# Kernel tuning notes

Measured on AMD Instinct MI355X. Metric: run time of the kernel, lower is better.

## Reference

```python
import jax, jax.numpy as jnp
import numpy as np

NUM_HEADS = 16


def setup_inputs() -> dict:
    key = jax.random.key(0)
    ks = jax.random.split(key, 7)
    T, B, E = 2048, 2, 1024
    return {
        "query": jax.random.normal(ks[0], (T, B, E), jnp.float32),
        "key": jax.random.normal(ks[1], (T, B, E), jnp.float32),
        "value": jax.random.normal(ks[2], (T, B, E), jnp.float32),
        "query_pos": jax.random.normal(ks[3], (T, B, E), jnp.float32),
        "key_pos": jax.random.normal(ks[4], (T, B, E), jnp.float32),
        "W": jax.random.normal(ks[5], (E, E), jnp.float32) * (1.0 / np.sqrt(E)),
        "b": jax.random.normal(ks[6], (E,), jnp.float32) * 0.01,
    }


def reference(query, key, value, query_pos, key_pos, W, b):
    T, B, E = query.shape
    S = key.shape[0]
    H = NUM_HEADS
    D = E // H
    scale = jnp.asarray(D ** 0.5, query.dtype)

    identity = query  # residual uses query BEFORE positional add
    q = query + query_pos
    k = key + key_pos

    # (T,B,E) -> (B,H,T,D)
    q = q.reshape(T, B, H, D).transpose(1, 2, 0, 3)
    k = k.reshape(S, B, H, D).transpose(1, 2, 0, 3)
    v = value.reshape(S, B, H, D).transpose(1, 2, 0, 3)

    attn = jnp.einsum("bhtd,bhsd->bhts", q, k) / scale
    attn = jax.nn.softmax(attn, axis=-1)  # dropout p=0 -> identity

    out = jnp.einsum("bhts,bhsd->bhtd", attn, v)
    out = out.transpose(2, 0, 1, 3).reshape(T, B, E)  # (B,H,T,D)->(T,B,E)
    out = out @ W.T + b  # fuse_heads linear; out_dropout p=0 -> identity
    out = out + identity

    attn_avg = attn.sum(axis=1) / H  # average over heads -> (B,T,S)
    return out, attn_avg
```

## Files before the change

kernel.cpp:

```cpp
#include <hip/hip_runtime.h>

#define T_DIM 2048
#define S_DIM 2048
#define B_DIM 2
#define E_DIM 1024
#define H_DIM 16
#define D_DIM 64
#define MSHIFT 20.0f

typedef unsigned short u16;
typedef unsigned int u32;
typedef float v4f __attribute__((ext_vector_type(4)));
typedef short v8s __attribute__((ext_vector_type(8)));

__device__ __forceinline__ u16 f2bf(float f) {
    union { float f; u32 u; } x; x.f = f;
    return (u16)((x.u + 0x7fffu + ((x.u >> 16) & 1u)) >> 16);
}
__device__ __forceinline__ u16 f2bfr(float f) {
    union { float f; u32 u; } x; x.f = f;
    return (u16)((x.u + 0x8000u) >> 16);
}
__device__ __forceinline__ v4f mfma16(v8s a, v8s b, v4f c) {
    return __builtin_amdgcn_mfma_f32_16x16x32_bf16(a, b, c, 0, 0, 0);
}
__device__ __forceinline__ v8s ld8(const u16* p) {
    return *reinterpret_cast<const v8s*>(p);
}

__global__ __launch_bounds__(256) void prep_qk(
    const float* __restrict__ q, const float* __restrict__ qp,
    const float* __restrict__ k, const float* __restrict__ kp,
    u16* __restrict__ qb, u16* __restrict__ ks) {
    int o = blockIdx.x * 256 + threadIdx.x;
    int d = o & 63, t = (o >> 6) & 2047, h = (o >> 17) & 15, b = o >> 21;
    int src = ((t * B_DIM + b) << 10) + (h << 6) + d;
    qb[o] = f2bf(q[src] + qp[src]);
    ks[o] = f2bf(k[src] + kp[src]);
}

__global__ __launch_bounds__(256) void prep_w(const float* __restrict__ W, u16* __restrict__ Wb) {
    int o = blockIdx.x * 256 + threadIdx.x;
    Wb[o] = f2bf(W[o]);
}

__global__ __launch_bounds__(256) void prep_vt(const float* __restrict__ V, u16* __restrict__ vt) {
    __shared__ float tile[64 * 65];
    int bx = blockIdx.x;
    int bh = bx >> 5;
    int s0 = (bx & 31) * 64;
    int b = bh >> 4, h = bh & 15;
    int tid = threadIdx.x;
    int quarter = tid >> 6, c = tid & 63;
    int boff = b * E_DIM + h * 64;
#pragma unroll
    for (int p = 0; p < 16; ++p) {
        int r = quarter * 16 + p;
        tile[r * 65 + c] = V[(size_t)(s0 + r) * (B_DIM * E_DIM) + boff + c];
    }
    __syncthreads();
#pragma unroll
    for (int p = 0; p < 16; ++p) {
        int d = quarter * 16 + p;
        vt[(size_t)bh * (D_DIM * S_DIM) + (size_t)d * S_DIM + s0 + c] = f2bf(tile[c * 65 + d]);
    }
}

#define PITCH 72
__global__ __launch_bounds__(256) void attn_pv(
    const u16* __restrict__ qb, const u16* __restrict__ ks, const u16* __restrict__ vt,
    float* __restrict__ lin, u16* __restrict__ Xb) {
    __shared__ u16 Kl[2][64 * PITCH];
    __shared__ u16 Vl[2][64 * PITCH];
    __shared__ u16 Pl[4][32 * PITCH];

    int bx = blockIdx.x;
    int bh = bx >> 4;
    int b = bh >> 4, h = bh & 15;
    int tid = threadIdx.x;
    int w = tid >> 6;
    int tbase = (bx & 15) * 128 + w * 32;
    int lane = tid & 63;
    int m = lane & 15, g = lane >> 4;

    int srow = tid >> 2;
    int sqtr = (tid & 3) * 16;

    uint4 kr0, kr1, vr0, vr1;
    auto load_stage = [&](int s0) {
        const uint4* kp = reinterpret_cast<const uint4*>(
            ks + ((size_t)bh * S_DIM + s0 + srow) * 64 + sqtr);
        kr0 = kp[0]; kr1 = kp[1];
        const uint4* vp = reinterpret_cast<const uint4*>(
            vt + (size_t)bh * (D_DIM * S_DIM) + (size_t)srow * S_DIM + s0 + sqtr);
        vr0 = vp[0]; vr1 = vp[1];
    };
    auto write_stage = [&](int buf) {
        uint4* kd = reinterpret_cast<uint4*>(&Kl[buf][srow * PITCH + sqtr]);
        kd[0] = kr0; kd[1] = kr1;
        uint4* vd = reinterpret_cast<uint4*>(&Vl[buf][srow * PITCH + sqtr]);
        vd[0] = vr0; vd[1] = vr1;
    };

    const u16* qrow = qb + ((size_t)bh * T_DIM + tbase + m) * 64 + g * 8;
    v8s aq[2][2];
    aq[0][0] = ld8(qrow);        aq[0][1] = ld8(qrow + 32);
    aq[1][0] = ld8(qrow + 1024); aq[1][1] = ld8(qrow + 1024 + 32);

    v4f O[2][4];
    float lacc[2][4];
#pragma unroll
    for (int tr = 0; tr < 2; ++tr) {
#pragma unroll
        for (int dd = 0; dd < 4; ++dd) O[tr][dd] = (v4f){0.f, 0.f, 0.f, 0.f};
#pragma unroll
        for (int r = 0; r < 4; ++r) lacc[tr][r] = 0.f;
    }

    load_stage(0);
    write_stage(0);
    load_stage(64);
    __syncthreads();

    u16* Pw = Pl[w];
    for (int it = 0; it < 32; ++it) {
        int buf = it & 1;
        const u16* Kb = Kl[buf];
        const u16* Vb = Vl[buf];
#pragma unroll
        for (int ss = 0; ss < 4; ++ss) {
            v8s kf0 = ld8(&Kb[(ss * 16 + m) * PITCH + g * 8]);
            v8s kf1 = ld8(&Kb[(ss * 16 + m) * PITCH + 32 + g * 8]);
#pragma unroll
            for (int tr = 0; tr < 2; ++tr) {
                v4f z = {0.f, 0.f, 0.f, 0.f};
                z = mfma16(aq[tr][0], kf0, z);
                z = mfma16(aq[tr][1], kf1, z);
#pragma unroll
                for (int r = 0; r < 4; ++r) {
                    float e = __expf(fmaf(z[r], 0.125f, -MSHIFT));
                    lacc[tr][r] += e;
                    Pw[(tr * 16 + g * 4 + r) * PITCH + ss * 16 + m] = f2bfr(e);
                }
            }
        }
        v8s ap[2][2];
#pragma unroll
        for (int tr = 0; tr < 2; ++tr) {
            ap[tr][0] = ld8(&Pw[(tr * 16 + m) * PITCH + g * 8]);
            ap[tr][1] = ld8(&Pw[(tr * 16 + m) * PITCH + 32 + g * 8]);
        }
#pragma unroll
        for (int dd = 0; dd < 4; ++dd) {
            v8s bv0 = ld8(&Vb[(dd * 16 + m) * PITCH + g * 8]);
            v8s bv1 = ld8(&Vb[(dd * 16 + m) * PITCH + 32 + g * 8]);
#pragma unroll
            for (int tr = 0; tr < 2; ++tr) {
                O[tr][dd] = mfma16(ap[tr][0], bv0, O[tr][dd]);
                O[tr][dd] = mfma16(ap[tr][1], bv1, O[tr][dd]);
            }
        }
        if (it + 1 < 32) {
            write_stage(buf ^ 1);
            if (it + 2 < 32) load_stage((it + 2) * 64);
        }
        __syncthreads();
    }

#pragma unroll
    for (int tr = 0; tr < 2; ++tr)
#pragma unroll
        for (int r = 0; r < 4; ++r) {
#pragma unroll
            for (int off = 1; off <= 8; off <<= 1)
                lacc[tr][r] += __shfl_xor(lacc[tr][r], off);
        }

#pragma unroll
    for (int tr = 0; tr < 2; ++tr)
#pragma unroll
        for (int r = 0; r < 4; ++r) {
            float linv = 1.0f / lacc[tr][r];
            int t = tbase + tr * 16 + g * 4 + r;
            if (m == 0) lin[(size_t)bh * T_DIM + t] = linv;
#pragma unroll
            for (int dd = 0; dd < 4; ++dd)
                Xb[((size_t)t * B_DIM + b) * E_DIM + h * 64 + dd * 16 + m] =
                    f2bf(O[tr][dd][r] * linv);
        }
}

__global__ __launch_bounds__(256) void attn_avg(
    const u16* __restrict__ qb, const u16* __restrict__ ks,
    const float* __restrict__ lin, float* __restrict__ out1) {
    __shared__ u16 Kl[2][128 * PITCH];
    int bx = blockIdx.x;
    int b = bx >> 8;
    int tt = (bx >> 4) & 15;
    int st = bx & 15;
    int tid = threadIdx.x;
    int w = tid >> 6;
    int tbase = tt * 128 + w * 32;
    int s0 = st * 128;
    int lane = tid & 63, m = lane & 15, g = lane >> 4;

    int srow = tid >> 1;
    int soff = (tid & 1) * 32;

    uint4 kr[4];
    auto load_stage = [&](int h) {
        const uint4* kp = reinterpret_cast<const uint4*>(
            ks + ((size_t)(b * 16 + h) * S_DIM + s0 + srow) * 64 + soff);
        kr[0] = kp[0]; kr[1] = kp[1]; kr[2] = kp[2]; kr[3] = kp[3];
    };
    auto write_stage = [&](int buf) {
        uint4* kd = reinterpret_cast<uint4*>(&Kl[buf][srow * PITCH + soff]);
        kd[0] = kr[0]; kd[1] = kr[1]; kd[2] = kr[2]; kd[3] = kr[3];
    };

    v4f AVG[2][8];
#pragma unroll
    for (int tr = 0; tr < 2; ++tr)
#pragma unroll
        for (int ss = 0; ss < 8; ++ss) AVG[tr][ss] = (v4f){0.f, 0.f, 0.f, 0.f};

    load_stage(0);
    write_stage(0);
    load_stage(1);
    __syncthreads();

    for (int h = 0; h < H_DIM; ++h) {
        int buf = h & 1;
        int bh = b * 16 + h;
        const u16* qrow = qb + ((size_t)bh * T_DIM + tbase + m) * 64 + g * 8;
        v8s aq[2][2];
        aq[0][0] = ld8(qrow);        aq[0][1] = ld8(qrow + 32);
        aq[1][0] = ld8(qrow + 1024); aq[1][1] = ld8(qrow + 1024 + 32);
        float liv[2][4];
#pragma unroll
        for (int tr = 0; tr < 2; ++tr)
#pragma unroll
            for (int r = 0; r < 4; ++r)
                liv[tr][r] = lin[(size_t)bh * T_DIM + tbase + tr * 16 + g * 4 + r] * (1.0f / 16.0f);

        const u16* Kb = Kl[buf];
#pragma unroll
        for (int ss = 0; ss < 8; ++ss) {
            v8s kf0 = ld8(&Kb[(ss * 16 + m) * PITCH + g * 8]);
            v8s kf1 = ld8(&Kb[(ss * 16 + m) * PITCH + 32 + g * 8]);
#pragma unroll
            for (int tr = 0; tr < 2; ++tr) {
                v4f z = {0.f, 0.f, 0.f, 0.f};
                z = mfma16(aq[tr][0], kf0, z);
                z = mfma16(aq[tr][1], kf1, z);
#pragma unroll
                for (int r = 0; r < 4; ++r)
                    AVG[tr][ss][r] += __expf(fmaf(z[r], 0.125f, -MSHIFT)) * liv[tr][r];
            }
        }
        if (h + 1 < H_DIM) {
            write_stage(buf ^ 1);
            if (h + 2 < H_DIM) load_stage(h + 2);
        }
        __syncthreads();
    }
#pragma unroll
    for (int tr = 0; tr < 2; ++tr)
#pragma unroll
        for (int ss = 0; ss < 8; ++ss)
#pragma unroll
            for (int r = 0; r < 4; ++r) {
                int t = tbase + tr * 16 + g * 4 + r;
                out1[((size_t)b * T_DIM + t) * S_DIM + s0 + ss * 16 + m] = AVG[tr][ss][r];
            }
}

__global__ __launch_bounds__(256) void linear_mfma(
    const u16* __restrict__ Xb, const u16* __restrict__ Wb,
    const float* __restrict__ bias, const float* __restrict__ query,
    float* __restrict__ out0) {
    __shared__ u16 Al[2][64 * PITCH];
    __shared__ u16 Wl[2][128 * PITCH];
    int bx = blockIdx.x;
    int it = bx >> 3, jt = bx & 7;
    int tid = threadIdx.x;
    int w = tid >> 6;
    int lane = tid & 63;
    int m = lane & 15, g = lane >> 4;

    int arow = tid >> 2, aq4 = (tid & 3) * 16;
    int wrow = tid >> 1, wh2 = (tid & 1) * 32;

    uint4 ar0, ar1, wr0, wr1, wr2, wr3;
    auto load_stage = [&](int k0) {
        const uint4* ap = reinterpret_cast<const uint4*>(
            Xb + (size_t)(it * 64 + arow) * E_DIM + k0 + aq4);
        ar0 = ap[0]; ar1 = ap[1];
        const uint4* wp = reinterpret_cast<const uint4*>(
            Wb + (size_t)(jt * 128 + wrow) * E_DIM + k0 + wh2);
        wr0 = wp[0]; wr1 = wp[1]; wr2 = wp[2]; wr3 = wp[3];
    };
    auto write_stage = [&](int buf) {
        uint4* ad = reinterpret_cast<uint4*>(&Al[buf][arow * PITCH + aq4]);
        ad[0] = ar0; ad[1] = ar1;
        uint4* wd = reinterpret_cast<uint4*>(&Wl[buf][wrow * PITCH + wh2]);
        wd[0] = wr0; wd[1] = wr1; wd[2] = wr2; wd[3] = wr3;
    };

    v4f acc[4][2];
#pragma unroll
    for (int tr = 0; tr < 4; ++tr)
#pragma unroll
        for (int nn = 0; nn < 2; ++nn) acc[tr][nn] = (v4f){0.f, 0.f, 0.f, 0.f};

    load_stage(0);
    write_stage(0);
    load_stage(64);
    __syncthreads();

    for (int itk = 0; itk < 16; ++itk) {
        int buf = itk & 1;
        const u16* Ab = Al[buf];
        const u16* Ws = Wl[buf];
        v8s af[4][2], wf[2][2];
#pragma unroll
        for (int tr = 0; tr < 4; ++tr) {
            af[tr][0] = ld8(&Ab[(tr * 16 + m) * PITCH + g * 8]);
            af[tr][1] = ld8(&Ab[(tr * 16 + m) * PITCH + 32 + g * 8]);
        }
#pragma unroll
        for (int nn = 0; nn < 2; ++nn) {
            wf[nn][0] = ld8(&Ws[((w * 2 + nn) * 16 + m) * PITCH + g * 8]);
            wf[nn][1] = ld8(&Ws[((w * 2 + nn) * 16 + m) * PITCH + 32 + g * 8]);
        }
#pragma unroll
        for (int tr = 0; tr < 4; ++tr)
#pragma unroll
            for (int nn = 0; nn < 2; ++nn) {
                acc[tr][nn] = mfma16(af[tr][0], wf[nn][0], acc[tr][nn]);
                acc[tr][nn] = mfma16(af[tr][1], wf[nn][1], acc[tr][nn]);
            }
        if (itk + 1 < 16) {
            write_stage(buf ^ 1);
            if (itk + 2 < 16) load_stage((itk + 2) * 64);
        }
        __syncthreads();
    }

#pragma unroll
    for (int tr = 0; tr < 4; ++tr)
#pragma unroll
        for (int nn = 0; nn < 2; ++nn) {
            int col = jt * 128 + (w * 2 + nn) * 16 + m;
            float bv = bias[col];
#pragma unroll
            for (int r = 0; r < 4; ++r) {
                int row = it * 64 + tr * 16 + g * 4 + r;
                out0[(size_t)row * E_DIM + col] =
                    acc[tr][nn][r] + bv + query[(size_t)row * E_DIM + col];
            }
        }
}

extern "C" void kernel_launch(void* const* d_in, const int* in_sizes, int n_in,
                              void* d_out, int out_size, void* d_ws, size_t ws_size,
                              hipStream_t stream) {
    const float* query = (const float*)d_in[0];
    const float* key   = (const float*)d_in[1];
    const float* value = (const float*)d_in[2];
    const float* qpos  = (const float*)d_in[3];
    const float* kpos  = (const float*)d_in[4];
    const float* W     = (const float*)d_in[5];
    const float* bias  = (const float*)d_in[6];

    char* ws = (char*)d_ws;
    u16*   qb  = (u16*)(ws);
    u16*   ks  = (u16*)(ws + (size_t)( 8u << 20));
    u16*   vt  = (u16*)(ws + (size_t)(16u << 20));
    u16*   Wb  = (u16*)(ws + (size_t)(24u << 20));
    float* lin = (float*)(ws + (size_t)(26u << 20));
    u16*   Xb  = (u16*)(ws + (size_t)(27u << 20));

    float* out0 = (float*)d_out;
    float* out1 = out0 + (size_t)T_DIM * B_DIM * E_DIM;

    prep_qk<<<(B_DIM * H_DIM * T_DIM * D_DIM) / 256, 256, 0, stream>>>(query, qpos, key, kpos, qb, ks);
    prep_w<<<(E_DIM * E_DIM) / 256, 256, 0, stream>>>(W, Wb);
    prep_vt<<<B_DIM * H_DIM * (S_DIM / 64), 256, 0, stream>>>(value, vt);
    attn_pv<<<B_DIM * H_DIM * (T_DIM / 128), 256, 0, stream>>>(qb, ks, vt, lin, Xb);
    attn_avg<<<B_DIM * (T_DIM / 128) * (S_DIM / 128), 256, 0, stream>>>(qb, ks, lin, out1);
    linear_mfma<<<(T_DIM * B_DIM / 64) * (E_DIM / 128), 256, 0, stream>>>(Xb, Wb, bias, query, out0);
}
```

Before: 294.6 us.

## Use exp2 intrinsic, halve attn_avg S-tile, prefetch next-head Q and norms

```diff
diff --git a/kernel.cpp b/kernel.cpp
--- a/kernel.cpp
+++ b/kernel.cpp
@@ -7,6 +7,9 @@
 #define H_DIM 16
 #define D_DIM 64
 #define MSHIFT 20.0f
+#define EXP2S 0.18033688f
+#define EXP2C -28.8539008f
+#define EXP2(x) __builtin_amdgcn_exp2f(x)
 
 typedef unsigned short u16;
 typedef unsigned int u32;
@@ -138,7 +141,7 @@
                 z = mfma16(aq[tr][1], kf1, z);
 #pragma unroll
                 for (int r = 0; r < 4; ++r) {
-                    float e = __expf(fmaf(z[r], 0.125f, -MSHIFT));
+                    float e = EXP2(fmaf(z[r], EXP2S, EXP2C));
                     lacc[tr][r] += e;
                     Pw[(tr * 16 + g * 4 + r) * PITCH + ss * 16 + m] = f2bfr(e);
                 }
@@ -190,72 +193,84 @@
         }
 }
 
-__global__ __launch_bounds__(256) void attn_avg(
+__global__ __launch_bounds__(256, 4) void attn_avg(
     const u16* __restrict__ qb, const u16* __restrict__ ks,
     const float* __restrict__ lin, float* __restrict__ out1) {
-    __shared__ u16 Kl[2][128 * PITCH];
+    __shared__ u16 Kl[2][64 * PITCH];
     int bx = blockIdx.x;
-    int b = bx >> 8;
-    int tt = (bx >> 4) & 15;
-    int st = bx & 15;
+    int b = bx >> 9;
+    int tt = (bx >> 5) & 15;
+    int st = bx & 31;
     int tid = threadIdx.x;
     int w = tid >> 6;
     int tbase = tt * 128 + w * 32;
-    int s0 = st * 128;
+    int sbase = st * 64;
     int lane = tid & 63, m = lane & 15, g = lane >> 4;
 
-    int srow = tid >> 1;
-    int soff = (tid & 1) * 32;
-
-    uint4 kr[4];
+    int srow = tid >> 2;
+    int sqtr = (tid & 3) * 16;
+
+    uint4 kr0, kr1;
     auto load_stage = [&](int h) {
         const uint4* kp = reinterpret_cast<const uint4*>(
-            ks + ((size_t)(b * 16 + h) * S_DIM + s0 + srow) * 64 + soff);
-        kr[0] = kp[0]; kr[1] = kp[1]; kr[2] = kp[2]; kr[3] = kp[3];
+            ks + ((size_t)(b * 16 + h) * S_DIM + sbase + srow) * 64 + sqtr);
+        kr0 = kp[0]; kr1 = kp[1];
     };
     auto write_stage = [&](int buf) {
-        uint4* kd = reinterpret_cast<uint4*>(&Kl[buf][srow * PITCH + soff]);
-        kd[0] = kr[0]; kd[1] = kr[1]; kd[2] = kr[2]; kd[3] = kr[3];
-    };
-
-    v4f AVG[2][8];
+        uint4* kd = reinterpret_cast<uint4*>(&Kl[buf][srow * PITCH + sqtr]);
+        kd[0] = kr0; kd[1] = kr1;
+    };
+
+    v8s aqc00, aqc01, aqc10, aqc11, aqn00, aqn01, aqn10, aqn11;
+    float livc[2][4], livn[2][4];
+    auto load_q = [&](int h, v8s& a00, v8s& a01, v8s& a10, v8s& a11, float (&liv)[2][4]) {
+        int bh = b * 16 + h;
+        const u16* qrow = qb + ((size_t)bh * T_DIM + tbase + m) * 64 + g * 8;
+        a00 = ld8(qrow);        a01 = ld8(qrow + 32);
+        a10 = ld8(qrow + 1024); a11 = ld8(qrow + 1024 + 32);
+#pragma unroll
+        for (int tr = 0; tr < 2; ++tr)
+#pragma unroll
+            for (int r = 0; r < 4; ++r)
+                liv[tr][r] = lin[(size_t)bh * T_DIM + tbase + tr * 16 + g * 4 + r] * (1.0f / 16.0f);
+    };
+
+    v4f AVG[2][4];
 #pragma unroll
     for (int tr = 0; tr < 2; ++tr)
 #pragma unroll
-        for (int ss = 0; ss < 8; ++ss) AVG[tr][ss] = (v4f){0.f, 0.f, 0.f, 0.f};
+        for (int ss = 0; ss < 4; ++ss) AVG[tr][ss] = (v4f){0.f, 0.f, 0.f, 0.f};
 
     load_stage(0);
     write_stage(0);
     load_stage(1);
+    load_q(0, aqc00, aqc01, aqc10, aqc11, livc);
     __syncthreads();
 
     for (int h = 0; h < H_DIM; ++h) {
         int buf = h & 1;
-        int bh = b * 16 + h;
-        const u16* qrow = qb + ((size_t)bh * T_DIM + tbase + m) * 64 + g * 8;
-        v8s aq[2][2];
-        aq[0][0] = ld8(qrow);        aq[0][1] = ld8(qrow + 32);
-        aq[1][0] = ld8(qrow + 1024); aq[1][1] = ld8(qrow + 1024 + 32);
-        float liv[2][4];
-#pragma unroll
-        for (int tr = 0; tr < 2; ++tr)
-#pragma unroll
-            for (int r = 0; r < 4; ++r)
-                liv[tr][r] = lin[(size_t)bh * T_DIM + tbase + tr * 16 + g * 4 + r] * (1.0f / 16.0f);
+        if (h + 1 < H_DIM) load_q(h + 1, aqn00, aqn01, aqn10, aqn11, livn);
 
         const u16* Kb = Kl[buf];
 #pragma unroll
-        for (int ss = 0; ss < 8; ++ss) {
+        for (int ss = 0; ss < 4; ++ss) {
             v8s kf0 = ld8(&Kb[(ss * 16 + m) * PITCH + g * 8]);
             v8s kf1 = ld8(&Kb[(ss * 16 + m) * PITCH + 32 + g * 8]);
-#pragma unroll
-            for (int tr = 0; tr < 2; ++tr) {
+            {
                 v4f z = {0.f, 0.f, 0.f, 0.f};
-                z = mfma16(aq[tr][0], kf0, z);
-                z = mfma16(aq[tr][1], kf1, z);
+                z = mfma16(aqc00, kf0, z);
+                z = mfma16(aqc01, kf1, z);
 #pragma unroll
                 for (int r = 0; r < 4; ++r)
-                    AVG[tr][ss][r] += __expf(fmaf(z[r], 0.125f, -MSHIFT)) * liv[tr][r];
+                    AVG[0][ss][r] += EXP2(fmaf(z[r], EXP2S, EXP2C)) * livc[0][r];
+            }
+            {
+                v4f z = {0.f, 0.f, 0.f, 0.f};
+                z = mfma16(aqc10, kf0, z);
+                z = mfma16(aqc11, kf1, z);
+#pragma unroll
+                for (int r = 0; r < 4; ++r)
+                    AVG[1][ss][r] += EXP2(fmaf(z[r], EXP2S, EXP2C)) * livc[1][r];
             }
         }
         if (h + 1 < H_DIM) {
@@ -263,15 +278,20 @@
             if (h + 2 < H_DIM) load_stage(h + 2);
         }
         __syncthreads();
+        aqc00 = aqn00; aqc01 = aqn01; aqc10 = aqn10; aqc11 = aqn11;
+#pragma unroll
+        for (int tr = 0; tr < 2; ++tr)
+#pragma unroll
+            for (int r = 0; r < 4; ++r) livc[tr][r] = livn[tr][r];
     }
 #pragma unroll
     for (int tr = 0; tr < 2; ++tr)
 #pragma unroll
-        for (int ss = 0; ss < 8; ++ss)
+        for (int ss = 0; ss < 4; ++ss)
 #pragma unroll
             for (int r = 0; r < 4; ++r) {
                 int t = tbase + tr * 16 + g * 4 + r;
-                out1[((size_t)b * T_DIM + t) * S_DIM + s0 + ss * 16 + m] = AVG[tr][ss][r];
+                out1[((size_t)b * T_DIM + t) * S_DIM + sbase + ss * 16 + m] = AVG[tr][ss][r];
             }
 }
 
@@ -388,6 +408,6 @@
     prep_w<<<(E_DIM * E_DIM) / 256, 256, 0, stream>>>(W, Wb);
     prep_vt<<<B_DIM * H_DIM * (S_DIM / 64), 256, 0, stream>>>(value, vt);
     attn_pv<<<B_DIM * H_DIM * (T_DIM / 128), 256, 0, stream>>>(qb, ks, vt, lin, Xb);
-    attn_avg<<<B_DIM * (T_DIM / 128) * (S_DIM / 128), 256, 0, stream>>>(qb, ks, lin, out1);
+    attn_avg<<<B_DIM * (T_DIM / 128) * (S_DIM / 64), 256, 0, stream>>>(qb, ks, lin, out1);
     linear_mfma<<<(T_DIM * B_DIM / 64) * (E_DIM / 128), 256, 0, stream>>>(Xb, Wb, bias, query, out0);
 }
```

Result: faster. 266.2 us (-9.6%).
